# Kernel tuning notes

Measured on AMD Instinct MI355X. Metric: run time of the kernel, lower is better.

Reference implementation:

```python
import jax, jax.numpy as jnp
import numpy as np

# Hyperparameters from init_kwargs
SIGMA = 0.01   # memristor conductance noise std
R = 1.0        # line resistance scale used in power accounting
WMAX1 = 1.0
WMAX2 = 1.0
B, C, H, W = 4, 3, 64, 64
K = 2                      # AvgPool2d kernel/stride
D1 = C * (H // K) * (W // K)   # 3072 flattened features after pooling
D2 = 2048
D3 = 1024


def setup_inputs() -> dict:
    key = jax.random.key(0)
    ks = jax.random.split(key, 4)
    x = jax.random.normal(ks[0], (B, C, H, W), jnp.float32)
    bias = jax.random.normal(ks[1], (C, H, W), jnp.float32) * 0.01
    W1 = jax.random.normal(ks[2], (D2, D1), jnp.float32) / np.float32(np.sqrt(D1))
    W2 = jax.random.normal(ks[3], (D3, D2), jnp.float32) / np.float32(np.sqrt(D2))
    g1 = jnp.float32(1.0)  # learnt_Gmax[0], initialized to Wmax[0]
    g2 = jnp.float32(1.0)  # learnt_Gmax[1]
    return {"x": x, "bias": bias, "W1": W1, "W2": W2, "g1": g1, "g2": g2}


def reference(x, bias, W1, W2, g1, g2):
    # input bias (MemSE.input_bias=True)
    x = x + bias[None]
    b = x.shape[0]
    eye2 = jnp.eye(D2, dtype=x.dtype)
    eye3 = jnp.eye(D3, dtype=x.dtype)

    # --- AvgPool2d(2,2): gamma is still empty at this point, only mean pooled ---
    x = x.reshape(b, C, H // K, K, W // K, K).mean(axis=(3, 5))
    x = x.reshape(b, -1)                        # [B, D1]

    # --- Linear 1: crossbar noise injection (gamma empty -> created here) ---
    c1 = g1 / WMAX1                             # conductance scaling G = c * W
    mu = x @ W1.T                               # [B, D2] mean propagation
    m2 = x * x                                  # E[x^2] (gamma == 0 before this layer)
    # two conductance arrays (pos/neg) each with iid noise var sigma^2, output /c
    vn1 = 2.0 * (SIGMA / c1) ** 2 * jnp.sum(m2, axis=-1)        # [B]
    gamma = vn1[:, None, None] * eye2[None]                      # [B, D2, D2]
    P_tot = (c1 / R) * jnp.einsum('oi,bi->b', jnp.abs(W1), m2)   # crossbar power

    # --- Softplus: first-order moment propagation (Jacobian = sigmoid(mu)) ---
    d = jax.nn.sigmoid(mu)                      # [B, D2]
    gamma = gamma * d[:, :, None] * d[:, None, :]
    mu = jax.nn.softplus(mu)

    # --- Linear 2: full covariance propagation W gamma W^T + noise diag ---
    c2 = g2 / WMAX2
    mu2 = mu @ W2.T                             # [B, D3]
    tmp = jnp.einsum('oi,bij->boj', W2, gamma)  # [B, D3, D2]
    gamma2 = jnp.einsum('boj,pj->bop', tmp, W2) # [B, D3, D3]
    m2b = mu * mu + jnp.diagonal(gamma, axis1=1, axis2=2)        # E[x^2]
    vn2 = 2.0 * (SIGMA / c2) ** 2 * jnp.sum(m2b, axis=-1)
    gamma2 = gamma2 + vn2[:, None, None] * eye3[None]
    P_tot = P_tot + (c2 / R) * jnp.einsum('oi,bi->b', jnp.abs(W2), m2b)

    return mu2, gamma2, P_tot
```

## Files before the change

### kernel.cpp

```cpp
#include <hip/hip_runtime.h>
#include <hip/hip_bf16.h>
#include <cstdint>

#define SIGMA 0.01f

constexpr int D1 = 3072;
constexpr int D2 = 2048;
constexpr int D3 = 1024;

typedef __bf16 bf16x8 __attribute__((ext_vector_type(8)));
typedef float f32x4 __attribute__((ext_vector_type(4)));

#define GLOAD16(gp, lp) \
  __builtin_amdgcn_global_load_lds((const __attribute__((address_space(1))) void*)(gp), \
                                   (__attribute__((address_space(3))) void*)(lp), 16, 0, 0)

__global__ void pool_kernel(const float* __restrict__ x, const float* __restrict__ bias,
                            float* __restrict__ pooled, float* __restrict__ Spart) {
  int idx = blockIdx.x * 256 + threadIdx.x;
  int b = idx / D1;
  int r = idx % D1;
  int c = r >> 10;
  int oh = (r >> 5) & 31;
  int ow = r & 31;
  int xb = ((b * 3 + c) * 64 + oh * 2) * 64 + ow * 2;
  int bb = (c * 64 + oh * 2) * 64 + ow * 2;
  float v = 0.25f * ((x[xb] + bias[bb]) + (x[xb + 1] + bias[bb + 1]) +
                     (x[xb + 64] + bias[bb + 64]) + (x[xb + 65] + bias[bb + 65]));
  pooled[idx] = v;
  float s = v * v;
  #pragma unroll
  for (int off = 32; off; off >>= 1) s += __shfl_down(s, off, 64);
  __shared__ float wsum[4];
  if ((threadIdx.x & 63) == 0) wsum[threadIdx.x >> 6] = s;
  __syncthreads();
  if (threadIdx.x == 0) Spart[blockIdx.x] = wsum[0] + wsum[1] + wsum[2] + wsum[3];
}

__global__ void lin1_kernel(const float* __restrict__ pooled, const float* __restrict__ W1,
                            float* __restrict__ mu, float* __restrict__ Pp1) {
  int o = blockIdx.x, tid = threadIdx.x;
  const float4* wrow = (const float4*)(W1 + (size_t)o * D1);
  const float4* p4 = (const float4*)pooled;
  float acc[4] = {0, 0, 0, 0}, pab[4] = {0, 0, 0, 0};
  #pragma unroll
  for (int it = 0; it < 3; it++) {
    int i4 = tid + it * 256;
    float4 w = wrow[i4];
    float ax = fabsf(w.x), ay = fabsf(w.y), az = fabsf(w.z), aw2 = fabsf(w.w);
    #pragma unroll
    for (int b = 0; b < 4; b++) {
      float4 p = p4[b * 768 + i4];
      acc[b] += w.x * p.x + w.y * p.y + w.z * p.z + w.w * p.w;
      pab[b] += ax * p.x * p.x + ay * p.y * p.y + az * p.z * p.z + aw2 * p.w * p.w;
    }
  }
  __shared__ float red[8][4];
  #pragma unroll
  for (int v = 0; v < 8; v++) {
    float s = (v < 4) ? acc[v] : pab[v - 4];
    #pragma unroll
    for (int off = 32; off; off >>= 1) s += __shfl_down(s, off, 64);
    if ((tid & 63) == 0) red[v][tid >> 6] = s;
  }
  __syncthreads();
  if (tid < 8) {
    float s = red[tid][0] + red[tid][1] + red[tid][2] + red[tid][3];
    if (tid < 4) mu[tid * D2 + o] = s;
    else Pp1[(size_t)(tid - 4) * D2 + o] = s;
  }
}

__global__ void act_kernel(const float* __restrict__ mu, const float* __restrict__ Spart,
                           const float* __restrict__ Pp1, const float* __restrict__ g1p,
                           float* __restrict__ musp, float* __restrict__ dscale,
                           float* __restrict__ m2b, float* __restrict__ Tpart,
                           float* __restrict__ P1q) {
  int bid = blockIdx.x, tid = threadIdx.x;
  int b = bid >> 2, q = bid & 3;
  float c1 = g1p[0];
  float sp0 = (tid < 12) ? Spart[b * 12 + tid] : 0.f;
  #pragma unroll
  for (int off = 32; off; off >>= 1) sp0 += __shfl_down(sp0, off, 64);
  __shared__ float ssb;
  if (tid == 0) ssb = sp0;
  __syncthreads();
  float vn1 = 2.0f * (SIGMA / c1) * (SIGMA / c1) * ssb;
  float sv = sqrtf(vn1);
  float ts = 0.f, ps = 0.f;
  #pragma unroll
  for (int it = 0; it < 2; it++) {
    int j = q * 512 + it * 256 + tid;
    int gj = b * D2 + j;
    float m = mu[gj];
    float d = 1.0f / (1.0f + expf(-m));
    float sp = fmaxf(m, 0.f) + log1pf(expf(-fabsf(m)));
    float mm = sp * sp + vn1 * d * d;
    musp[gj] = sp;
    dscale[gj] = sv * d;
    m2b[gj] = mm;
    ts += mm;
    ps += Pp1[gj];
  }
  __shared__ float red[2][4];
  #pragma unroll
  for (int v = 0; v < 2; v++) {
    float s = (v == 0) ? ts : ps;
    #pragma unroll
    for (int off = 32; off; off >>= 1) s += __shfl_down(s, off, 64);
    if ((tid & 63) == 0) red[v][tid >> 6] = s;
  }
  __syncthreads();
  if (tid == 0) {
    Tpart[bid] = red[0][0] + red[0][1] + red[0][2] + red[0][3];
    P1q[bid] = c1 * (red[1][0] + red[1][1] + red[1][2] + red[1][3]);
  }
}

__global__ void lin2_prep_kernel(const float* __restrict__ W2, const float* __restrict__ musp,
                                 const float* __restrict__ dscale, const float* __restrict__ m2b,
                                 __bf16* __restrict__ E, float* __restrict__ mu2,
                                 float* __restrict__ Pp2) {
  int o = blockIdx.x, tid = threadIdx.x;
  const float* wrow = W2 + (size_t)o * D2;
  int j0 = tid * 8;
  float w[8];
  *(float4*)&w[0] = *(const float4*)(wrow + j0);
  *(float4*)&w[4] = *(const float4*)(wrow + j0 + 4);
  float acc[4], pab[4];
  #pragma unroll
  for (int b = 0; b < 4; b++) {
    const float* ms = musp + b * D2 + j0;
    const float* dsc = dscale + b * D2 + j0;
    const float* mb = m2b + b * D2 + j0;
    bf16x8 ev;
    float a = 0.f, p = 0.f;
    #pragma unroll
    for (int jj = 0; jj < 8; jj++) {
      ev[jj] = (__bf16)(w[jj] * dsc[jj]);
      a += w[jj] * ms[jj];
      p += fabsf(w[jj]) * mb[jj];
    }
    *(bf16x8*)(E + ((size_t)b * D3 + o) * D2 + j0) = ev;
    acc[b] = a;
    pab[b] = p;
  }
  __shared__ float red[8][4];
  #pragma unroll
  for (int v = 0; v < 8; v++) {
    float s = (v < 4) ? acc[v] : pab[v - 4];
    #pragma unroll
    for (int off = 32; off; off >>= 1) s += __shfl_down(s, off, 64);
    if ((tid & 63) == 0) red[v][tid >> 6] = s;
  }
  __syncthreads();
  if (tid < 8) {
    float s = red[tid][0] + red[tid][1] + red[tid][2] + red[tid][3];
    if (tid < 4) mu2[tid * D3 + o] = s;
    else Pp2[(size_t)(tid - 4) * D3 + o] = s;
  }
}

__global__ __launch_bounds__(256, 4) void gamma2_gemm(const __bf16* __restrict__ E,
                                                      const float* __restrict__ Tpart,
                                                      const float* __restrict__ P1q,
                                                      const float* __restrict__ Pp2,
                                                      const float* __restrict__ g2p,
                                                      float* __restrict__ gamma2,
                                                      float* __restrict__ Ptot) {
  int bid = blockIdx.x;
  int tid = threadIdx.x;
  int wid = tid >> 6, lane = tid & 63;
  float c2 = g2p[0];

  if (bid == 0) {
    float s = 0.f;
    for (int k = lane; k < D3; k += 64) s += Pp2[(size_t)wid * D3 + k];
    #pragma unroll
    for (int off = 32; off; off >>= 1) s += __shfl_down(s, off, 64);
    if (lane == 0) {
      float p1 = P1q[wid * 4] + P1q[wid * 4 + 1] + P1q[wid * 4 + 2] + P1q[wid * 4 + 3];
      Ptot[wid] = p1 + c2 * s;
    }
  }

  int xcd = bid & 7, r = bid >> 3;
  int b = xcd >> 1;
  int tm = ((xcd & 1) << 3) | (r & 7);
  int tn = r >> 3;
  float vn2 = 2.0f * (SIGMA / c2) * (SIGMA / c2) *
              (Tpart[b * 4] + Tpart[b * 4 + 1] + Tpart[b * 4 + 2] + Tpart[b * 4 + 3]);

  __shared__ __bf16 As[4096];
  __shared__ __bf16 Bs[4096];
  char* AsB = (char*)As;
  char* BsB = (char*)Bs;

  int wr = wid >> 1, wc = wid & 1;
  int srow = ((tid >> 7) << 4) | ((tid >> 2) & 15);
  int sc = (((tid >> 6) & 1) << 2) | (tid & 3);
  const __bf16* Eb = E + (size_t)b * D3 * D2;
  const __bf16* gA = Eb + (size_t)(tm * 64 + srow) * D2 + sc * 8;
  const __bf16* gB = Eb + (size_t)(tn * 64 + srow) * D2 + sc * 8;
  unsigned dst0 = (unsigned)wid * 1024u;

  int fr = lane & 15, kg = lane >> 4;
  unsigned po = ((unsigned)(fr << 2) | (unsigned)kg) << 4;
  unsigned a0off = (unsigned)((wr * 2 + 0) << 11) + po;
  unsigned a1off = (unsigned)((wr * 2 + 1) << 11) + po;
  unsigned b0off = (unsigned)((wc * 2 + 0) << 11) + po;
  unsigned b1off = (unsigned)((wc * 2 + 1) << 11) + po;

  f32x4 acc[2][2] = {};

  for (int k0 = 0; k0 < D2; k0 += 64) {
    GLOAD16(gA + k0,           AsB + dst0);
    GLOAD16(gA + k0 + 32 * D2, AsB + 4096 + dst0);
    GLOAD16(gB + k0,           BsB + dst0);
    GLOAD16(gB + k0 + 32 * D2, BsB + 4096 + dst0);
    __syncthreads();
    #pragma unroll
    for (int ks = 0; ks < 2; ks++) {
      unsigned kso = (unsigned)ks << 10;
      bf16x8 a0 = *(const bf16x8*)(AsB + a0off + kso);
      bf16x8 a1 = *(const bf16x8*)(AsB + a1off + kso);
      bf16x8 b0 = *(const bf16x8*)(BsB + b0off + kso);
      bf16x8 b1 = *(const bf16x8*)(BsB + b1off + kso);
      acc[0][0] = __builtin_amdgcn_mfma_f32_16x16x32_bf16(a0, b0, acc[0][0], 0, 0, 0);
      acc[0][1] = __builtin_amdgcn_mfma_f32_16x16x32_bf16(a0, b1, acc[0][1], 0, 0, 0);
      acc[1][0] = __builtin_amdgcn_mfma_f32_16x16x32_bf16(a1, b0, acc[1][0], 0, 0, 0);
      acc[1][1] = __builtin_amdgcn_mfma_f32_16x16x32_bf16(a1, b1, acc[1][1], 0, 0, 0);
    }
    __syncthreads();
  }

  float* outb = gamma2 + (size_t)b * D3 * D3;
  int row0 = tm * 64 + wr * 32 + kg * 4;
  int col0 = tn * 64 + wc * 32 + fr;
  #pragma unroll
  for (int mi = 0; mi < 2; mi++)
    #pragma unroll
    for (int ni = 0; ni < 2; ni++)
      #pragma unroll
      for (int rg = 0; rg < 4; rg++) {
        int row = row0 + mi * 16 + rg;
        int cc = col0 + ni * 16;
        float v = acc[mi][ni][rg];
        if (row == cc) v += vn2;
        outb[(size_t)row * D3 + cc] = v;
      }
}

extern "C" void kernel_launch(void* const* d_in, const int* in_sizes, int n_in,
                              void* d_out, int out_size, void* d_ws, size_t ws_size,
                              hipStream_t stream) {
  (void)in_sizes; (void)n_in; (void)out_size; (void)ws_size;
  const float* x    = (const float*)d_in[0];
  const float* bias = (const float*)d_in[1];
  const float* W1   = (const float*)d_in[2];
  const float* W2   = (const float*)d_in[3];
  const float* g1   = (const float*)d_in[4];
  const float* g2   = (const float*)d_in[5];
  float* out = (float*)d_out;

  float* ws     = (float*)d_ws;
  float* pooled = ws;
  float* mu     = pooled + 4 * D1;
  float* musp   = mu + 4 * D2;
  float* dscale = musp + 4 * D2;
  float* m2b    = dscale + 4 * D2;
  float* Pp1    = m2b + 4 * D2;
  float* Pp2    = Pp1 + 4 * D2;
  float* Spart  = Pp2 + 4 * D3;
  float* Tpart  = Spart + 48;
  float* P1q    = Tpart + 16;
  size_t used = (size_t)(4 * D1 + 6 * 4 * D2 + 4 * D3 + 80) * 4;
  size_t eoff = (used + 255) / 256 * 256;
  __bf16* E = (__bf16*)((char*)d_ws + eoff);

  pool_kernel<<<48, 256, 0, stream>>>(x, bias, pooled, Spart);
  lin1_kernel<<<2048, 256, 0, stream>>>(pooled, W1, mu, Pp1);
  act_kernel<<<16, 256, 0, stream>>>(mu, Spart, Pp1, g1, musp, dscale, m2b, Tpart, P1q);
  lin2_prep_kernel<<<1024, 256, 0, stream>>>(W2, musp, dscale, m2b, E, out, Pp2);
  gamma2_gemm<<<1024, 256, 0, stream>>>(E, Tpart, P1q, Pp2, g2, out + 4 * D3,
                                        out + 4 * D3 + (size_t)4 * D3 * D3);
}
```

Measured before the change: 60.32 us.

## Fuse activation into lin1 epilogue and move reductions into gamma2 GEMM

```diff
diff --git a/kernel.cpp b/kernel.cpp
--- a/kernel.cpp
+++ b/kernel.cpp
@@ -38,7 +38,9 @@
 }
 
 __global__ void lin1_kernel(const float* __restrict__ pooled, const float* __restrict__ W1,
-                            float* __restrict__ mu, float* __restrict__ Pp1) {
+                            const float* __restrict__ Spart, const float* __restrict__ g1p,
+                            float* __restrict__ musp, float* __restrict__ dscale,
+                            float* __restrict__ m2b, float* __restrict__ Pp1) {
   int o = blockIdx.x, tid = threadIdx.x;
   const float4* wrow = (const float4*)(W1 + (size_t)o * D1);
   const float4* p4 = (const float4*)pooled;
@@ -66,54 +68,21 @@
   __syncthreads();
   if (tid < 8) {
     float s = red[tid][0] + red[tid][1] + red[tid][2] + red[tid][3];
-    if (tid < 4) mu[tid * D2 + o] = s;
-    else Pp1[(size_t)(tid - 4) * D2 + o] = s;
-  }
-}
-
-__global__ void act_kernel(const float* __restrict__ mu, const float* __restrict__ Spart,
-                           const float* __restrict__ Pp1, const float* __restrict__ g1p,
-                           float* __restrict__ musp, float* __restrict__ dscale,
-                           float* __restrict__ m2b, float* __restrict__ Tpart,
-                           float* __restrict__ P1q) {
-  int bid = blockIdx.x, tid = threadIdx.x;
-  int b = bid >> 2, q = bid & 3;
-  float c1 = g1p[0];
-  float sp0 = (tid < 12) ? Spart[b * 12 + tid] : 0.f;
-  #pragma unroll
-  for (int off = 32; off; off >>= 1) sp0 += __shfl_down(sp0, off, 64);
-  __shared__ float ssb;
-  if (tid == 0) ssb = sp0;
-  __syncthreads();
-  float vn1 = 2.0f * (SIGMA / c1) * (SIGMA / c1) * ssb;
-  float sv = sqrtf(vn1);
-  float ts = 0.f, ps = 0.f;
-  #pragma unroll
-  for (int it = 0; it < 2; it++) {
-    int j = q * 512 + it * 256 + tid;
-    int gj = b * D2 + j;
-    float m = mu[gj];
-    float d = 1.0f / (1.0f + expf(-m));
-    float sp = fmaxf(m, 0.f) + log1pf(expf(-fabsf(m)));
-    float mm = sp * sp + vn1 * d * d;
-    musp[gj] = sp;
-    dscale[gj] = sv * d;
-    m2b[gj] = mm;
-    ts += mm;
-    ps += Pp1[gj];
-  }
-  __shared__ float red[2][4];
-  #pragma unroll
-  for (int v = 0; v < 2; v++) {
-    float s = (v == 0) ? ts : ps;
-    #pragma unroll
-    for (int off = 32; off; off >>= 1) s += __shfl_down(s, off, 64);
-    if ((tid & 63) == 0) red[v][tid >> 6] = s;
-  }
-  __syncthreads();
-  if (tid == 0) {
-    Tpart[bid] = red[0][0] + red[0][1] + red[0][2] + red[0][3];
-    P1q[bid] = c1 * (red[1][0] + red[1][1] + red[1][2] + red[1][3]);
+    if (tid < 4) {
+      int b = tid;
+      float ss = 0.f;
+      #pragma unroll
+      for (int i = 0; i < 12; i++) ss += Spart[b * 12 + i];
+      float c1 = g1p[0];
+      float vn1 = 2.0f * (SIGMA / c1) * (SIGMA / c1) * ss;
+      float d = 1.0f / (1.0f + expf(-s));
+      float sp = fmaxf(s, 0.f) + log1pf(expf(-fabsf(s)));
+      musp[b * D2 + o] = sp;
+      dscale[b * D2 + o] = sqrtf(vn1) * d;
+      m2b[b * D2 + o] = sp * sp + vn1 * d * d;
+    } else {
+      Pp1[(size_t)(tid - 4) * D2 + o] = s;
+    }
   }
 }
 
@@ -162,70 +131,87 @@
 }
 
 __global__ __launch_bounds__(256, 4) void gamma2_gemm(const __bf16* __restrict__ E,
-                                                      const float* __restrict__ Tpart,
-                                                      const float* __restrict__ P1q,
+                                                      const float* __restrict__ m2b,
+                                                      const float* __restrict__ Pp1,
                                                       const float* __restrict__ Pp2,
+                                                      const float* __restrict__ g1p,
                                                       const float* __restrict__ g2p,
                                                       float* __restrict__ gamma2,
                                                       float* __restrict__ Ptot) {
-  int bid = blockIdx.x;
-  int tid = threadIdx.x;
+  int bid = blockIdx.x, tid = threadIdx.x;
   int wid = tid >> 6, lane = tid & 63;
+  int wr = wid >> 1, wc = wid & 1;
   float c2 = g2p[0];
-
-  if (bid == 0) {
-    float s = 0.f;
-    for (int k = lane; k < D3; k += 64) s += Pp2[(size_t)wid * D3 + k];
-    #pragma unroll
-    for (int off = 32; off; off >>= 1) s += __shfl_down(s, off, 64);
-    if (lane == 0) {
-      float p1 = P1q[wid * 4] + P1q[wid * 4 + 1] + P1q[wid * 4 + 2] + P1q[wid * 4 + 3];
-      Ptot[wid] = p1 + c2 * s;
-    }
-  }
 
   int xcd = bid & 7, r = bid >> 3;
   int b = xcd >> 1;
-  int tm = ((xcd & 1) << 3) | (r & 7);
-  int tn = r >> 3;
-  float vn2 = 2.0f * (SIGMA / c2) * (SIGMA / c2) *
-              (Tpart[b * 4] + Tpart[b * 4 + 1] + Tpart[b * 4 + 2] + Tpart[b * 4 + 3]);
-
-  __shared__ __bf16 As[4096];
-  __shared__ __bf16 Bs[4096];
+  int t = r * 2 + (xcd & 1);
+  int tm = t >> 4, tn = t & 15;
+
+  __shared__ __bf16 As[4096], Bs[4096];
+  __shared__ float vred[4], pred1[4], pred2[4];
+  __shared__ float vn2sh;
+
+  {
+    float s = 0.f;
+    #pragma unroll
+    for (int i = 0; i < 8; i++) s += m2b[b * D2 + tid + i * 256];
+    #pragma unroll
+    for (int off = 32; off; off >>= 1) s += __shfl_down(s, off, 64);
+    if (lane == 0) vred[wid] = s;
+  }
+  if (bid < 4) {
+    float p1s = 0.f, p2s = 0.f;
+    #pragma unroll
+    for (int i = 0; i < 8; i++) p1s += Pp1[(size_t)bid * D2 + tid + i * 256];
+    #pragma unroll
+    for (int i = 0; i < 4; i++) p2s += Pp2[(size_t)bid * D3 + tid + i * 256];
+    #pragma unroll
+    for (int off = 32; off; off >>= 1) {
+      p1s += __shfl_down(p1s, off, 64);
+      p2s += __shfl_down(p2s, off, 64);
+    }
+    if (lane == 0) { pred1[wid] = p1s; pred2[wid] = p2s; }
+  }
+  __syncthreads();
+  if (tid == 0) {
+    vn2sh = 2.0f * (SIGMA / c2) * (SIGMA / c2) * (vred[0] + vred[1] + vred[2] + vred[3]);
+    if (bid < 4)
+      Ptot[bid] = g1p[0] * (pred1[0] + pred1[1] + pred1[2] + pred1[3]) +
+                  c2 * (pred2[0] + pred2[1] + pred2[2] + pred2[3]);
+  }
+
+  int rb = wid >> 1, ks = wid & 1;
+  int srow = rb * 16 + (lane & 15);
+  int skof = ks * 32 + ((lane >> 4) << 3);
+  const __bf16* Eb = E + (size_t)b * D3 * D2;
+  const __bf16* gA = Eb + (size_t)(tm * 64 + srow) * D2 + skof;
+  const __bf16* gB = Eb + (size_t)(tn * 64 + srow) * D2 + skof;
   char* AsB = (char*)As;
   char* BsB = (char*)Bs;
-
-  int wr = wid >> 1, wc = wid & 1;
-  int srow = ((tid >> 7) << 4) | ((tid >> 2) & 15);
-  int sc = (((tid >> 6) & 1) << 2) | (tid & 3);
-  const __bf16* Eb = E + (size_t)b * D3 * D2;
-  const __bf16* gA = Eb + (size_t)(tm * 64 + srow) * D2 + sc * 8;
-  const __bf16* gB = Eb + (size_t)(tn * 64 + srow) * D2 + sc * 8;
-  unsigned dst0 = (unsigned)wid * 1024u;
-
-  int fr = lane & 15, kg = lane >> 4;
-  unsigned po = ((unsigned)(fr << 2) | (unsigned)kg) << 4;
-  unsigned a0off = (unsigned)((wr * 2 + 0) << 11) + po;
-  unsigned a1off = (unsigned)((wr * 2 + 1) << 11) + po;
-  unsigned b0off = (unsigned)((wc * 2 + 0) << 11) + po;
-  unsigned b1off = (unsigned)((wc * 2 + 1) << 11) + po;
+  unsigned dstA = (unsigned)wid * 1024u;
+
+  unsigned lo = (unsigned)lane * 16u;
+  unsigned a0base = (unsigned)(wr * 4) * 1024u + lo;
+  unsigned a1base = (unsigned)(wr * 4 + 2) * 1024u + lo;
+  unsigned b0base = (unsigned)(wc * 4) * 1024u + lo;
+  unsigned b1base = (unsigned)(wc * 4 + 2) * 1024u + lo;
 
   f32x4 acc[2][2] = {};
 
   for (int k0 = 0; k0 < D2; k0 += 64) {
-    GLOAD16(gA + k0,           AsB + dst0);
-    GLOAD16(gA + k0 + 32 * D2, AsB + 4096 + dst0);
-    GLOAD16(gB + k0,           BsB + dst0);
-    GLOAD16(gB + k0 + 32 * D2, BsB + 4096 + dst0);
+    GLOAD16(gA + k0,           AsB + dstA);
+    GLOAD16(gA + k0 + 32 * D2, AsB + 4096 + dstA);
+    GLOAD16(gB + k0,           BsB + dstA);
+    GLOAD16(gB + k0 + 32 * D2, BsB + 4096 + dstA);
     __syncthreads();
     #pragma unroll
-    for (int ks = 0; ks < 2; ks++) {
-      unsigned kso = (unsigned)ks << 10;
-      bf16x8 a0 = *(const bf16x8*)(AsB + a0off + kso);
-      bf16x8 a1 = *(const bf16x8*)(AsB + a1off + kso);
-      bf16x8 b0 = *(const bf16x8*)(BsB + b0off + kso);
-      bf16x8 b1 = *(const bf16x8*)(BsB + b1off + kso);
+    for (int ks2 = 0; ks2 < 2; ks2++) {
+      unsigned kso = (unsigned)ks2 << 10;
+      bf16x8 a0 = *(const bf16x8*)(AsB + a0base + kso);
+      bf16x8 a1 = *(const bf16x8*)(AsB + a1base + kso);
+      bf16x8 b0 = *(const bf16x8*)(BsB + b0base + kso);
+      bf16x8 b1 = *(const bf16x8*)(BsB + b1base + kso);
       acc[0][0] = __builtin_amdgcn_mfma_f32_16x16x32_bf16(a0, b0, acc[0][0], 0, 0, 0);
       acc[0][1] = __builtin_amdgcn_mfma_f32_16x16x32_bf16(a0, b1, acc[0][1], 0, 0, 0);
       acc[1][0] = __builtin_amdgcn_mfma_f32_16x16x32_bf16(a1, b0, acc[1][0], 0, 0, 0);
@@ -234,7 +220,9 @@
     __syncthreads();
   }
 
+  float vn2 = vn2sh;
   float* outb = gamma2 + (size_t)b * D3 * D3;
+  int fr = lane & 15, kg = lane >> 4;
   int row0 = tm * 64 + wr * 32 + kg * 4;
   int col0 = tn * 64 + wc * 32 + fr;
   #pragma unroll
@@ -265,23 +253,19 @@
 
   float* ws     = (float*)d_ws;
   float* pooled = ws;
-  float* mu     = pooled + 4 * D1;
-  float* musp   = mu + 4 * D2;
+  float* musp   = pooled + 4 * D1;
   float* dscale = musp + 4 * D2;
   float* m2b    = dscale + 4 * D2;
   float* Pp1    = m2b + 4 * D2;
   float* Pp2    = Pp1 + 4 * D2;
   float* Spart  = Pp2 + 4 * D3;
-  float* Tpart  = Spart + 48;
-  float* P1q    = Tpart + 16;
-  size_t used = (size_t)(4 * D1 + 6 * 4 * D2 + 4 * D3 + 80) * 4;
+  size_t used = (size_t)(4 * D1 + 4 * 4 * D2 + 4 * D3 + 64) * 4;
   size_t eoff = (used + 255) / 256 * 256;
   __bf16* E = (__bf16*)((char*)d_ws + eoff);
 
   pool_kernel<<<48, 256, 0, stream>>>(x, bias, pooled, Spart);
-  lin1_kernel<<<2048, 256, 0, stream>>>(pooled, W1, mu, Pp1);
-  act_kernel<<<16, 256, 0, stream>>>(mu, Spart, Pp1, g1, musp, dscale, m2b, Tpart, P1q);
+  lin1_kernel<<<2048, 256, 0, stream>>>(pooled, W1, Spart, g1, musp, dscale, m2b, Pp1);
   lin2_prep_kernel<<<1024, 256, 0, stream>>>(W2, musp, dscale, m2b, E, out, Pp2);
-  gamma2_gemm<<<1024, 256, 0, stream>>>(E, Tpart, P1q, Pp2, g2, out + 4 * D3,
+  gamma2_gemm<<<1024, 256, 0, stream>>>(E, m2b, Pp1, Pp2, g1, g2, out + 4 * D3,
                                         out + 4 * D3 + (size_t)4 * D3 * D3);
 }
```

After: 90.35 us. 49.8% more time.
